# Optimization experiments

Hardware: AMD Instinct MI355X
Metric: run time of the kernel (lower is better)

The kernel has to match this reference:

```python
import jax, jax.numpy as jnp
import numpy as np

C = 256
CQK = C // 8  # 32

def setup_inputs() -> dict:
    key = jax.random.key(0)
    ks = jax.random.split(key, 8)
    N, L = 8, 4096
    x = jax.random.normal(ks[0], (N, C, L), dtype=jnp.float32)
    s = 1.0 / np.sqrt(C)
    Wq = jax.random.normal(ks[1], (CQK, C), dtype=jnp.float32) * s
    bq = jnp.zeros((CQK,), dtype=jnp.float32)
    Wk = jax.random.normal(ks[2], (CQK, C), dtype=jnp.float32) * s
    bk = jnp.zeros((CQK,), dtype=jnp.float32)
    Wv = jax.random.normal(ks[3], (C, C), dtype=jnp.float32) * s
    bv = jnp.zeros((C,), dtype=jnp.float32)
    gamma = jnp.ones((1,), dtype=jnp.float32) * 0.5  # nonzero so output depends on attention
    return {"x": x, "Wq": Wq, "bq": bq, "Wk": Wk, "bk": bk, "Wv": Wv, "bv": bv, "gamma": gamma}

def reference(x, Wq, bq, Wk, bk, Wv, bv, gamma):
    # conv1d with kernel_size=1 == pointwise linear over channel dim
    q = jnp.einsum('ncl,oc->nol', x, Wq) + bq[None, :, None]   # (N, C/8, L)
    k = jnp.einsum('ncl,oc->nol', x, Wk) + bk[None, :, None]   # (N, C/8, L)
    v = jnp.einsum('ncl,oc->nol', x, Wv) + bv[None, :, None]   # (N, C, L)
    # energy[n, i, j] = q[n, :, i] . k[n, :, j]
    energy = jnp.einsum('nci,ncj->nij', q, k)                  # (N, L, L)
    attention = jax.nn.softmax(energy, axis=-1)
    # out[n, c, i] = sum_j v[n, c, j] * attention[n, i, j]
    out = jnp.einsum('ncj,nij->nci', v, attention)             # (N, C, L)
    return gamma * out + x
```

## Files before the change

kernel.cpp:

```cpp
#include <hip/hip_runtime.h>
#include <hip/hip_bf16.h>

#define NB 8
#define CC 256
#define LL 4096
#define CQ 32

typedef __bf16 bf16x8 __attribute__((ext_vector_type(8)));
typedef float f32x4 __attribute__((ext_vector_type(4)));
typedef unsigned short u16x4 __attribute__((ext_vector_type(4)));

union B8u { bf16x8 b; u16x4 h[2]; };
union P4u { u16x4 u; __bf16 e[4]; };

#define WS_QT  ((size_t)0)
#define WS_KT  ((size_t)1048576)
#define WS_VV  ((size_t)2097152)
#define WS_WQ  ((size_t)18874368)
#define WS_BQ  ((size_t)18882560)
#define WS_WK  ((size_t)18882592)
#define WS_BK  ((size_t)18890784)
#define WS_WV  ((size_t)18890816)
#define WS_BV  ((size_t)18956352)

__device__ __forceinline__ bool tag_is_bf16(const void* gamma_raw) {
  return *(const unsigned short*)gamma_raw != 0;
}
__device__ __forceinline__ float cvt_load(const void* p, size_t i, bool b16) {
  return b16 ? (float)((const __bf16*)p)[i] : ((const float*)p)[i];
}

__global__ __launch_bounds__(256) void convert_wb_kernel(
    const void* __restrict__ Wq, const void* __restrict__ bq,
    const void* __restrict__ Wk, const void* __restrict__ bk,
    const void* __restrict__ Wv, const void* __restrict__ bv,
    const void* __restrict__ gm, __bf16* __restrict__ ws)
{
  const bool b16 = tag_is_bf16(gm);
  int t = blockIdx.x * 256 + threadIdx.x;
  for (int i = t; i < 82240; i += 32 * 256) {
    float v; size_t dof;
    if (i < 8192)       { v = cvt_load(Wq, i, b16);         dof = WS_WQ + i; }
    else if (i < 8224)  { v = cvt_load(bq, i - 8192, b16);  dof = WS_BQ + (i - 8192); }
    else if (i < 16416) { v = cvt_load(Wk, i - 8224, b16);  dof = WS_WK + (i - 8224); }
    else if (i < 16448) { v = cvt_load(bk, i - 16416, b16); dof = WS_BK + (i - 16416); }
    else if (i < 81984) { v = cvt_load(Wv, i - 16448, b16); dof = WS_WV + (i - 16448); }
    else                { v = cvt_load(bv, i - 81984, b16); dof = WS_BV + (i - 81984); }
    ws[dof] = (__bf16)v;
  }
}

__global__ __launch_bounds__(256, 2) void proj_kernel(
    const void* __restrict__ x_raw, const void* __restrict__ gm_raw,
    __bf16* __restrict__ ws)
{
  const bool b16 = tag_is_bf16(gm_raw);
  const int bid = blockIdx.x;
  const int n = bid & 7, l0 = (bid >> 3) * 64;
  const int tid = threadIdx.x;
  const int w = tid >> 6, lane = tid & 63, li = lane & 15, qd = lane >> 4;

  __shared__ __align__(16) char xlt[64 * 512];

  {
    const int g = tid & 31, h = tid >> 5;
    B8u rv[8];
    #pragma unroll
    for (int ci = 0; ci < 8; ++ci) {
      const int c = g * 8 + ci;
      const size_t goff = (size_t)n * CC * LL + (size_t)c * LL + l0 + h * 8;
      if (b16) {
        rv[ci].b = *(const bf16x8*)((const __bf16*)x_raw + goff);
      } else {
        const float* xf0 = (const float*)x_raw + goff;
        f32x4 a = *(const f32x4*)xf0;
        f32x4 b = *(const f32x4*)(xf0 + 4);
        #pragma unroll
        for (int s = 0; s < 4; ++s) {
          rv[ci].b[s] = (__bf16)a[s]; rv[ci].b[s + 4] = (__bf16)b[s];
        }
      }
    }
    #pragma unroll
    for (int s = 0; s < 8; ++s) {
      bf16x8 wv;
      #pragma unroll
      for (int ci = 0; ci < 8; ++ci) wv[ci] = rv[ci].b[s];
      const int l = h * 8 + s;
      *(bf16x8*)(xlt + (size_t)l * 512 + ((16 * g) ^ (s << 4))) = wv;
    }
  }
  __syncthreads();

  const __bf16* Wqk = (w < 2) ? (ws + WS_WQ) : (ws + WS_WK);
  const __bf16* Wv  = ws + WS_WV;
  const int obase = (w & 1) * 16;

  f32x4 vacc[4][4];
  f32x4 qkacc[4];
  #pragma unroll
  for (int a = 0; a < 4; ++a) {
    qkacc[a] = f32x4{0, 0, 0, 0};
    #pragma unroll
    for (int b = 0; b < 4; ++b) vacc[a][b] = f32x4{0, 0, 0, 0};
  }

  for (int k0 = 0; k0 < CC; k0 += 32) {
    bf16x8 xf[4];
    #pragma unroll
    for (int lt = 0; lt < 4; ++lt) {
      const int l = lt * 16 + li;
      xf[lt] = *(const bf16x8*)(xlt + (size_t)l * 512
                 + (((k0 + qd * 8) * 2) ^ ((li & 7) << 4)));
    }
    bf16x8 wa = *(const bf16x8*)(Wqk + (size_t)(obase + li) * CC + k0 + qd * 8);
    #pragma unroll
    for (int lt = 0; lt < 4; ++lt)
      qkacc[lt] = __builtin_amdgcn_mfma_f32_16x16x32_bf16(wa, xf[lt], qkacc[lt], 0, 0, 0);
    #pragma unroll
    for (int ct = 0; ct < 4; ++ct) {
      bf16x8 wb = *(const bf16x8*)(Wv + (size_t)(w * 64 + ct * 16 + li) * CC + k0 + qd * 8);
      #pragma unroll
      for (int lt = 0; lt < 4; ++lt)
        vacc[lt][ct] = __builtin_amdgcn_mfma_f32_16x16x32_bf16(xf[lt], wb, vacc[lt][ct], 0, 0, 0);
    }
  }

  {
    const __bf16* bqk = (w < 2) ? (ws + WS_BQ) : (ws + WS_BK);
    __bf16* dqk = ((w < 2) ? (ws + WS_QT) : (ws + WS_KT)) + (size_t)n * LL * CQ;
    float bf[4];
    #pragma unroll
    for (int rr = 0; rr < 4; ++rr) bf[rr] = (float)bqk[obase + qd * 4 + rr];
    #pragma unroll
    for (int lt = 0; lt < 4; ++lt) {
      P4u pk;
      #pragma unroll
      for (int rr = 0; rr < 4; ++rr) pk.e[rr] = (__bf16)(qkacc[lt][rr] + bf[rr]);
      *(u16x4*)(dqk + (size_t)(l0 + lt * 16 + li) * CQ + obase + qd * 4) = pk.u;
    }
  }
  {
    __bf16* dv = ws + WS_VV + (size_t)n * 128 * CC * 32;
    #pragma unroll
    for (int ct = 0; ct < 4; ++ct) {
      int c = w * 64 + ct * 16 + li;
      float bvf = (float)(ws + WS_BV)[c];
      #pragma unroll
      for (int lt = 0; lt < 4; ++lt) {
        int jl = lt * 16 + qd * 4;
        int jb = (l0 + jl) >> 5, jj = jl & 31;
        P4u pk;
        #pragma unroll
        for (int rr = 0; rr < 4; ++rr) pk.e[rr] = (__bf16)(vacc[lt][ct][rr] + bvf);
        *(u16x4*)(dv + ((size_t)jb * CC + c) * 32 + jj) = pk.u;
      }
    }
  }
}

__global__ __launch_bounds__(1024, 4) void attn_kernel(
    const __bf16* __restrict__ ws, const void* __restrict__ x_raw,
    const void* __restrict__ gamma_raw, void* __restrict__ out_raw)
{
  const int bid = blockIdx.x;
  const int n = bid & 7, iblk = (bid >> 3) * 128;
  const int tid = threadIdx.x, w = tid >> 6, lane = tid & 63;
  const int li = lane & 15, qd = lane >> 4;
  const int it = w & 7, jh = w >> 3;
  const int cg = w & 7, jg = w >> 3;

  const __bf16* qtn = ws + WS_QT + (size_t)n * LL * CQ;
  const __bf16* ktn = ws + WS_KT + (size_t)n * LL * CQ;
  const __bf16* v2n = ws + WS_VV + (size_t)n * 128 * CC * 32;

  __shared__ __align__(16) __bf16 plds[2][4][8][16][36];
  __shared__ __align__(16) float  lbuf[16][16];
  __shared__ __align__(16) __bf16 olds[256][72];
  float* scratch = (float*)&plds[0][0][0][0][0];

  bf16x8 qfrag = *(const bf16x8*)(qtn + (size_t)(iblk + it * 16 + li) * CQ + qd * 8);
  const f32x4 zero = {0.f, 0.f, 0.f, 0.f};

  f32x4 oacc[16];
  #pragma unroll
  for (int t = 0; t < 16; ++t) oacc[t] = zero;
  float lp = 0.f;

  bf16x8 kf[4];
  #pragma unroll
  for (int u = 0; u < 4; ++u)
    kf[u] = *(const bf16x8*)(ktn + (size_t)(jh * 64 + u * 16 + li) * CQ + qd * 8);

  for (int js = 0; js < LL; js += 128) {
    const int buf = (js >> 7) & 1;
    bf16x8 vf[4];
    #pragma unroll
    for (int s = 0; s < 2; ++s) {
      const int jb = (js >> 5) + jg * 2 + s;
      #pragma unroll
      for (int ct = 0; ct < 2; ++ct)
        vf[s * 2 + ct] = *(const bf16x8*)(v2n + ((size_t)jb * CC + cg * 32 + ct * 16 + li) * 32 + qd * 8);
    }
    #pragma unroll
    for (int u = 0; u < 4; ++u) {
      f32x4 s = __builtin_amdgcn_mfma_f32_16x16x32_bf16(kf[u], qfrag, zero, 0, 0, 0);
      P4u pk;
      #pragma unroll
      for (int r = 0; r < 4; ++r) {
        float e = __expf(s[r]); lp += e; pk.e[r] = (__bf16)e;
      }
      *(u16x4*)(&plds[buf][jh * 2 + (u >> 1)][it][li][(u & 1) * 16 + qd * 4]) = pk.u;
    }
    {
      const int jn = (js + 128 < LL) ? (js + 128) : 0;
      #pragma unroll
      for (int u = 0; u < 4; ++u)
        kf[u] = *(const bf16x8*)(ktn + (size_t)(jn + jh * 64 + u * 16 + li) * CQ + qd * 8);
    }
    __syncthreads();
    #pragma unroll
    for (int s = 0; s < 2; ++s) {
      #pragma unroll
      for (int tt = 0; tt < 8; ++tt) {
        B8u ap;
        ap.b = *(const bf16x8*)(&plds[buf][jg * 2 + s][tt][li][qd * 8]);
        oacc[tt * 2 + 0] = __builtin_amdgcn_mfma_f32_16x16x32_bf16(ap.b, vf[s * 2 + 0], oacc[tt * 2 + 0], 0, 0, 0);
        oacc[tt * 2 + 1] = __builtin_amdgcn_mfma_f32_16x16x32_bf16(ap.b, vf[s * 2 + 1], oacc[tt * 2 + 1], 0, 0, 0);
      }
    }
  }

  lp += __shfl_xor(lp, 16);
  lp += __shfl_xor(lp, 32);
  lbuf[it * 2 + jh][li] = lp;
  __syncthreads();

  #pragma unroll
  for (int r = 0; r < 2; ++r) {
    if (jg == 1 && (cg >> 2) == r) {
      float* d = scratch + (size_t)(cg & 3) * 4096;
      #pragma unroll
      for (int t = 0; t < 16; ++t)
        *(f32x4*)(d + t * 256 + lane * 4) = oacc[t];
    }
    __syncthreads();
    if (jg == 0 && (cg >> 2) == r) {
      const float* s = scratch + (size_t)(cg & 3) * 4096;
      #pragma unroll
      for (int t = 0; t < 16; ++t)
        oacc[t] += *(const f32x4*)(s + t * 256 + lane * 4);
    }
    __syncthreads();
  }

  const bool b16 = tag_is_bf16(gamma_raw);
  const float gma = b16 ? (float)(*(const __bf16*)gamma_raw)
                        : (*(const float*)gamma_raw);

  f32x4 gi[8];
  if (jg == 0) {
    #pragma unroll
    for (int pp = 0; pp < 8; ++pp) {
      f32x4 l0v = *(const f32x4*)(&lbuf[pp * 2 + 0][qd * 4]);
      f32x4 l1v = *(const f32x4*)(&lbuf[pp * 2 + 1][qd * 4]);
      #pragma unroll
      for (int rr = 0; rr < 4; ++rr) gi[pp][rr] = gma / (l0v[rr] + l1v[rr]);
    }
  }

  const int ec = tid >> 5, i2 = (tid & 31) * 2;
  #pragma unroll
  for (int h = 0; h < 2; ++h) {
    if (jg == 0) {
      #pragma unroll
      for (int pi = 0; pi < 4; ++pi) {
        const int pp = h * 4 + pi;
        #pragma unroll
        for (int ct = 0; ct < 2; ++ct) {
          P4u pk;
          #pragma unroll
          for (int rr = 0; rr < 4; ++rr)
            pk.e[rr] = (__bf16)(oacc[pp * 2 + ct][rr] * gi[pp][rr]);
          *(u16x4*)(&olds[cg * 32 + ct * 16 + li][pi * 16 + qd * 4]) = pk.u;
        }
      }
    }
    __syncthreads();
    const int ibase = iblk + h * 64;
    if (b16) {
      const __bf16* xn = (const __bf16*)x_raw + (size_t)n * CC * LL;
      __bf16* outn = (__bf16*)out_raw + (size_t)n * CC * LL;
      for (int c = ec; c < CC; c += 32) {
        unsigned int ov = *(const unsigned int*)(&olds[c][i2]);
        unsigned int xv = *(const unsigned int*)(xn + (size_t)c * LL + ibase + i2);
        const __bf16* op = (const __bf16*)&ov;
        const __bf16* xp = (const __bf16*)&xv;
        unsigned int res;
        __bf16* rp = (__bf16*)&res;
        rp[0] = (__bf16)((float)op[0] + (float)xp[0]);
        rp[1] = (__bf16)((float)op[1] + (float)xp[1]);
        *(unsigned int*)(outn + (size_t)c * LL + ibase + i2) = res;
      }
    } else {
      const float* xn = (const float*)x_raw + (size_t)n * CC * LL;
      float* outn = (float*)out_raw + (size_t)n * CC * LL;
      for (int c = ec; c < CC; c += 32) {
        unsigned int ov = *(const unsigned int*)(&olds[c][i2]);
        const __bf16* op = (const __bf16*)&ov;
        float2 xv = *(const float2*)(xn + (size_t)c * LL + ibase + i2);
        float2 res;
        res.x = (float)op[0] + xv.x;
        res.y = (float)op[1] + xv.y;
        *(float2*)(outn + (size_t)c * LL + ibase + i2) = res;
      }
    }
    __syncthreads();
  }
}

extern "C" void kernel_launch(void* const* d_in, const int* in_sizes, int n_in,
                              void* d_out, int out_size, void* d_ws, size_t ws_size,
                              hipStream_t stream) {
  (void)in_sizes; (void)n_in; (void)out_size; (void)ws_size;
  __bf16* ws = (__bf16*)d_ws;

  hipLaunchKernelGGL(convert_wb_kernel, dim3(32), dim3(256), 0, stream,
                     d_in[1], d_in[2], d_in[3], d_in[4], d_in[5], d_in[6],
                     d_in[7], ws);
  hipLaunchKernelGGL(proj_kernel, dim3(512), dim3(256), 0, stream,
                     d_in[0], d_in[7], ws);
  hipLaunchKernelGGL(attn_kernel, dim3(256), dim3(1024), 0, stream,
                     (const __bf16*)ws, d_in[0], d_in[7], d_out);
}
```

Baseline: 196.7 us.

## Switch PV product to 32x32x16 MFMA with split V loads around barrier

Replaces the 16x16x32 MFMA tiles in the attention-times-V accumulation with 32x32x16 MFMA tiles, remapping the waves to (i-group, channel-group, j-half) and re-indexing the probability buffer and V loads. The barrier is moved earlier, and the second half of the V fragments is loaded after it and interleaved with the first half's MFMAs, so the next K fetch overlaps compute. The epilogue reduction and normalization are rewritten for the 32x32 accumulator layout, with per-row inverse sums precomputed into shared memory. This aims to cut LDS reads per flop and raise matrix-core efficiency. The cost is more complex index mapping and possibly higher register pressure.

After: 274.9 us. 1.4x slower.

```diff
diff --git a/kernel.cpp b/kernel.cpp
--- a/kernel.cpp
+++ b/kernel.cpp
@@ -8,6 +8,7 @@
 
 typedef __bf16 bf16x8 __attribute__((ext_vector_type(8)));
 typedef float f32x4 __attribute__((ext_vector_type(4)));
+typedef float f32x16 __attribute__((ext_vector_type(16)));
 typedef unsigned short u16x4 __attribute__((ext_vector_type(4)));
 
 union B8u { bf16x8 b; u16x4 h[2]; };
@@ -167,8 +168,9 @@
   const int n = bid & 7, iblk = (bid >> 3) * 128;
   const int tid = threadIdx.x, w = tid >> 6, lane = tid & 63;
   const int li = lane & 15, qd = lane >> 4;
+  const int cl = lane & 31, hi = lane >> 5;
   const int it = w & 7, jh = w >> 3;
-  const int cg = w & 7, jg = w >> 3;
+  const int ig = w & 1, cgc = (w >> 1) & 3, jg = w >> 3;
 
   const __bf16* qtn = ws + WS_QT + (size_t)n * LL * CQ;
   const __bf16* ktn = ws + WS_KT + (size_t)n * LL * CQ;
@@ -176,16 +178,24 @@
 
   __shared__ __align__(16) __bf16 plds[2][4][8][16][36];
   __shared__ __align__(16) float  lbuf[16][16];
+  __shared__ __align__(16) float  linv[128];
   __shared__ __align__(16) __bf16 olds[256][72];
   float* scratch = (float*)&plds[0][0][0][0][0];
+  const char* pbase = (const char*)&plds[0][0][0][0][0];
 
   bf16x8 qfrag = *(const bf16x8*)(qtn + (size_t)(iblk + it * 16 + li) * CQ + qd * 8);
   const f32x4 zero = {0.f, 0.f, 0.f, 0.f};
-
-  f32x4 oacc[16];
-  #pragma unroll
-  for (int t = 0; t < 16; ++t) oacc[t] = zero;
+  const f32x16 z16 = {0.f,0.f,0.f,0.f, 0.f,0.f,0.f,0.f,
+                      0.f,0.f,0.f,0.f, 0.f,0.f,0.f,0.f};
+
+  f32x16 acc[2][2];
+  acc[0][0] = z16; acc[0][1] = z16; acc[1][0] = z16; acc[1][1] = z16;
   float lp = 0.f;
+
+  const unsigned abase = (unsigned)jg * 18432 + (unsigned)(ig * 4 + (cl >> 4)) * 1152
+                       + (unsigned)(cl & 15) * 72 + (unsigned)hi * 16;
+  const size_t vco0 = (size_t)(cgc * 64 + cl) * 32 + hi * 8;
+  const size_t vco1 = (size_t)(cgc * 64 + 32 + cl) * 32 + hi * 8;
 
   bf16x8 kf[4];
   #pragma unroll
@@ -194,13 +204,12 @@
 
   for (int js = 0; js < LL; js += 128) {
     const int buf = (js >> 7) & 1;
-    bf16x8 vf[4];
+    const size_t jbb = (size_t)((js >> 5) + jg * 2);
+    bf16x8 vfA[4];
     #pragma unroll
     for (int s = 0; s < 2; ++s) {
-      const int jb = (js >> 5) + jg * 2 + s;
-      #pragma unroll
-      for (int ct = 0; ct < 2; ++ct)
-        vf[s * 2 + ct] = *(const bf16x8*)(v2n + ((size_t)jb * CC + cg * 32 + ct * 16 + li) * 32 + qd * 8);
+      vfA[s * 2 + 0] = *(const bf16x8*)(v2n + jbb * CC * 32 + vco0 + s * 16);
+      vfA[s * 2 + 1] = *(const bf16x8*)(v2n + jbb * CC * 32 + vco1 + s * 16);
     }
     #pragma unroll
     for (int u = 0; u < 4; ++u) {
@@ -212,22 +221,37 @@
       }
       *(u16x4*)(&plds[buf][jh * 2 + (u >> 1)][it][li][(u & 1) * 16 + qd * 4]) = pk.u;
     }
+    __syncthreads();
+    const char* pb = pbase + buf * 36864;
+    bf16x8 vfB[4];
+    #pragma unroll
+    for (int s = 0; s < 2; ++s) {
+      vfB[s * 2 + 0] = *(const bf16x8*)(v2n + (jbb + 1) * CC * 32 + vco0 + s * 16);
+      vfB[s * 2 + 1] = *(const bf16x8*)(v2n + (jbb + 1) * CC * 32 + vco1 + s * 16);
+    }
+    #pragma unroll
+    for (int s = 0; s < 2; ++s) {
+      const bf16x8 ap0 = *(const bf16x8*)(pb + abase + 0 * 2304 + s * 32);
+      const bf16x8 ap1 = *(const bf16x8*)(pb + abase + 1 * 2304 + s * 32);
+      acc[0][0] = __builtin_amdgcn_mfma_f32_32x32x16_bf16(ap0, vfA[s * 2 + 0], acc[0][0], 0, 0, 0);
+      acc[0][1] = __builtin_amdgcn_mfma_f32_32x32x16_bf16(ap0, vfA[s * 2 + 1], acc[0][1], 0, 0, 0);
+      acc[1][0] = __builtin_amdgcn_mfma_f32_32x32x16_bf16(ap1, vfA[s * 2 + 0], acc[1][0], 0, 0, 0);
+      acc[1][1] = __builtin_amdgcn_mfma_f32_32x32x16_bf16(ap1, vfA[s * 2 + 1], acc[1][1], 0, 0, 0);
+    }
     {
       const int jn = (js + 128 < LL) ? (js + 128) : 0;
       #pragma unroll
       for (int u = 0; u < 4; ++u)
         kf[u] = *(const bf16x8*)(ktn + (size_t)(jn + jh * 64 + u * 16 + li) * CQ + qd * 8);
     }
-    __syncthreads();
     #pragma unroll
     for (int s = 0; s < 2; ++s) {
-      #pragma unroll
-      for (int tt = 0; tt < 8; ++tt) {
-        B8u ap;
-        ap.b = *(const bf16x8*)(&plds[buf][jg * 2 + s][tt][li][qd * 8]);
-        oacc[tt * 2 + 0] = __builtin_amdgcn_mfma_f32_16x16x32_bf16(ap.b, vf[s * 2 + 0], oacc[tt * 2 + 0], 0, 0, 0);
-        oacc[tt * 2 + 1] = __builtin_amdgcn_mfma_f32_16x16x32_bf16(ap.b, vf[s * 2 + 1], oacc[tt * 2 + 1], 0, 0, 0);
-      }
+      const bf16x8 ap0 = *(const bf16x8*)(pb + abase + 9216 + 0 * 2304 + s * 32);
+      const bf16x8 ap1 = *(const bf16x8*)(pb + abase + 9216 + 1 * 2304 + s * 32);
+      acc[0][0] = __builtin_amdgcn_mfma_f32_32x32x16_bf16(ap0, vfB[s * 2 + 0], acc[0][0], 0, 0, 0);
+      acc[0][1] = __builtin_amdgcn_mfma_f32_32x32x16_bf16(ap0, vfB[s * 2 + 1], acc[0][1], 0, 0, 0);
+      acc[1][0] = __builtin_amdgcn_mfma_f32_32x32x16_bf16(ap1, vfB[s * 2 + 0], acc[1][0], 0, 0, 0);
+      acc[1][1] = __builtin_amdgcn_mfma_f32_32x32x16_bf16(ap1, vfB[s * 2 + 1], acc[1][1], 0, 0, 0);
     }
   }
 
@@ -238,18 +262,34 @@
 
   #pragma unroll
   for (int r = 0; r < 2; ++r) {
-    if (jg == 1 && (cg >> 2) == r) {
-      float* d = scratch + (size_t)(cg & 3) * 4096;
-      #pragma unroll
-      for (int t = 0; t < 16; ++t)
-        *(f32x4*)(d + t * 256 + lane * 4) = oacc[t];
-    }
-    __syncthreads();
-    if (jg == 0 && (cg >> 2) == r) {
-      const float* s = scratch + (size_t)(cg & 3) * 4096;
-      #pragma unroll
-      for (int t = 0; t < 16; ++t)
-        oacc[t] += *(const f32x4*)(s + t * 256 + lane * 4);
+    if (jg == 1 && (cgc >> 1) == r) {
+      float* d = scratch + (size_t)(ig * 2 + (cgc & 1)) * 4096 + lane * 4;
+      #pragma unroll
+      for (int tl = 0; tl < 2; ++tl)
+        #pragma unroll
+        for (int ct = 0; ct < 2; ++ct)
+          #pragma unroll
+          for (int q = 0; q < 4; ++q) {
+            f32x4 v4 = { acc[tl][ct][q * 4 + 0], acc[tl][ct][q * 4 + 1],
+                         acc[tl][ct][q * 4 + 2], acc[tl][ct][q * 4 + 3] };
+            *(f32x4*)(d + (tl * 8 + ct * 4 + q) * 256) = v4;
+          }
+    }
+    __syncthreads();
+    if (jg == 0 && (cgc >> 1) == r) {
+      const float* s0 = scratch + (size_t)(ig * 2 + (cgc & 1)) * 4096 + lane * 4;
+      #pragma unroll
+      for (int tl = 0; tl < 2; ++tl)
+        #pragma unroll
+        for (int ct = 0; ct < 2; ++ct)
+          #pragma unroll
+          for (int q = 0; q < 4; ++q) {
+            const f32x4 v4 = *(const f32x4*)(s0 + (tl * 8 + ct * 4 + q) * 256);
+            acc[tl][ct][q * 4 + 0] += v4[0];
+            acc[tl][ct][q * 4 + 1] += v4[1];
+            acc[tl][ct][q * 4 + 2] += v4[2];
+            acc[tl][ct][q * 4 + 3] += v4[3];
+          }
     }
     __syncthreads();
   }
@@ -257,32 +297,31 @@
   const bool b16 = tag_is_bf16(gamma_raw);
   const float gma = b16 ? (float)(*(const __bf16*)gamma_raw)
                         : (*(const float*)gamma_raw);
-
-  f32x4 gi[8];
-  if (jg == 0) {
-    #pragma unroll
-    for (int pp = 0; pp < 8; ++pp) {
-      f32x4 l0v = *(const f32x4*)(&lbuf[pp * 2 + 0][qd * 4]);
-      f32x4 l1v = *(const f32x4*)(&lbuf[pp * 2 + 1][qd * 4]);
-      #pragma unroll
-      for (int rr = 0; rr < 4; ++rr) gi[pp][rr] = gma / (l0v[rr] + l1v[rr]);
-    }
-  }
+  if (tid < 128) {
+    const int t16 = tid >> 4, tl16 = tid & 15;
+    linv[tid] = gma / (lbuf[t16 * 2 + 0][tl16] + lbuf[t16 * 2 + 1][tl16]);
+  }
+  __syncthreads();
 
   const int ec = tid >> 5, i2 = (tid & 31) * 2;
   #pragma unroll
   for (int h = 0; h < 2; ++h) {
-    if (jg == 0) {
-      #pragma unroll
-      for (int pi = 0; pi < 4; ++pi) {
-        const int pp = h * 4 + pi;
+    if (jg == 0 && ig == h) {
+      #pragma unroll
+      for (int tl = 0; tl < 2; ++tl) {
         #pragma unroll
         for (int ct = 0; ct < 2; ++ct) {
-          P4u pk;
+          const int c = cgc * 64 + ct * 32 + cl;
           #pragma unroll
-          for (int rr = 0; rr < 4; ++rr)
-            pk.e[rr] = (__bf16)(oacc[pp * 2 + ct][rr] * gi[pp][rr]);
-          *(u16x4*)(&olds[cg * 32 + ct * 16 + li][pi * 16 + qd * 4]) = pk.u;
+          for (int g = 0; g < 4; ++g) {
+            const int iloc = tl * 32 + 8 * g + 4 * hi;
+            const f32x4 gv = *(const f32x4*)&linv[h * 64 + iloc];
+            P4u pk;
+            #pragma unroll
+            for (int rr = 0; rr < 4; ++rr)
+              pk.e[rr] = (__bf16)(acc[tl][ct][g * 4 + rr] * gv[rr]);
+            *(u16x4*)(&olds[c][iloc]) = pk.u;
+          }
         }
       }
     }
```
